# Performance work log

Measured on AMD Instinct MI355X. Metric: run time of the kernel, lower is better.

Reference implementation:

```python
import jax, jax.numpy as jnp
import numpy as np

N_NODES = 100000
N_EDGES = 1600000
D_IN, D_HID, D_OUT = 256, 128, 64


def setup_inputs() -> dict:
    key = jax.random.key(0)
    k = jax.random.split(key, 6)
    x = jax.random.normal(k[0], (N_NODES, D_IN), dtype=jnp.float32)
    edge_index = jax.random.randint(k[1], (2, N_EDGES), 0, N_NODES, dtype=jnp.int64)
    W1 = jax.random.normal(k[2], (D_IN, D_HID), dtype=jnp.float32) / np.sqrt(D_IN)
    b1 = jnp.zeros((D_HID,), dtype=jnp.float32)
    W2 = jax.random.normal(k[3], (D_HID, D_OUT), dtype=jnp.float32) / np.sqrt(D_HID)
    b2 = jnp.zeros((D_OUT,), dtype=jnp.float32)
    return {"x": x, "edge_index": edge_index, "W1": W1, "b1": b1, "W2": W2, "b2": b2}


def gcn_conv(x, W, b, src, dst, n):
    """PyG GCNConv: h = D^-1/2 (A+I) D^-1/2 (x W) + b, symmetric norm with self-loops."""
    h = x @ W                                           # [n, d_out]
    # degree from destination (col) index, +1 for the self-loop edge weight
    deg = jnp.ones((n,), x.dtype).at[dst].add(jnp.float32(1.0))
    dinv = jax.lax.rsqrt(deg)                           # deg >= 1, no inf
    norm = dinv[src] * dinv[dst]                        # [E]
    agg = jax.ops.segment_sum(h[src] * norm[:, None], dst, num_segments=n)
    agg = agg + h * (dinv * dinv)[:, None]              # self-loop contribution
    return agg + b


def reference(x, edge_index, W1, b1, W2, b2):
    src, dst = edge_index[0], edge_index[1]
    n = x.shape[0]
    h = gcn_conv(x, W1, b1, src, dst, n)
    h = jax.nn.relu(h)                                  # dropout is identity in eval mode
    out = gcn_conv(h, W2, b2, src, dst, n)
    return out
```

## Files before the change

kernel.cpp:

```cpp
#include <hip/hip_runtime.h>
#include <stdint.h>

typedef unsigned short u16;
typedef unsigned int u32;
typedef __bf16 bf16x8 __attribute__((ext_vector_type(8)));
typedef float floatx4 __attribute__((ext_vector_type(4)));

static __device__ __forceinline__ float bf2f(u16 u) {
  union { u32 i; float f; } v; v.i = ((u32)u) << 16; return v.f;
}
static __device__ __forceinline__ u16 f2bf(float f) {
  union { float f; u32 i; } v; v.f = f;
  u32 u = v.i;
  return (u16)((u + 0x7fffu + ((u >> 16) & 1u)) >> 16);
}

static __device__ __forceinline__ void gload_lds16(const void* g, void* l) {
  __builtin_amdgcn_global_load_lds(
      (const __attribute__((address_space(1))) void*)g,
      (__attribute__((address_space(3))) void*)l, 16, 0, 0);
}

__global__ void k_edgemode(const int* __restrict__ ei, int* __restrict__ flag) {
  int t = threadIdx.x;
  int v = ei[2 * t + 1];
  unsigned long long b = __ballot(v == 0);
  if (t == 0) *flag = (b == ~0ull) ? 1 : 0;
}

static __device__ __forceinline__ int edge_src(const int* ei, int E, int i, int m64) {
  return m64 ? ei[2 * (size_t)i] : ei[i];
}
static __device__ __forceinline__ int edge_dst(const int* ei, int E, int i, int m64) {
  return m64 ? ei[2 * (size_t)E + 2 * (size_t)i] : ei[(size_t)E + i];
}

__global__ void k_transpose(const float* __restrict__ W1, const float* __restrict__ W2,
                            u16* __restrict__ Wt1, u16* __restrict__ Wt2) {
  int i = blockIdx.x * 256 + threadIdx.x;
  if (i < 256 * 128) {
    int k = i >> 7, c = i & 127;
    Wt1[c * 256 + k] = f2bf(W1[i]);
  } else {
    int j = i - 256 * 128;
    if (j < 128 * 64) {
      int k = j >> 6, c = j & 63;
      Wt2[c * 128 + k] = f2bf(W2[j]);
    }
  }
}

#define CHUNK 2048

__global__ void k_count(const int* __restrict__ ei, int E, const int* __restrict__ flag,
                        int* __restrict__ bucket_cnt, int NB) {
  __shared__ int h[1024];
  const int t = threadIdx.x;
  for (int i = t; i < 1024; i += 256) h[i] = 0;
  __syncthreads();
  const int c0 = blockIdx.x * CHUNK;
  const int cnt = min(CHUNK, E - c0);
  const int m64 = *flag;
  for (int i = t; i < cnt; i += 256)
    atomicAdd(&h[edge_dst(ei, E, c0 + i, m64) >> 7], 1);
  __syncthreads();
  for (int i = t; i < NB; i += 256)
    if (h[i]) atomicAdd(&bucket_cnt[i], h[i]);
}

__global__ void k_bscan(const int* __restrict__ bucket_cnt, int* __restrict__ bucket_base,
                        int* __restrict__ bucket_cursor, int NB,
                        int* __restrict__ row_ptr, int n, int E) {
  __shared__ int ts[256];
  const int t = threadIdx.x;
  const int b4 = t * 4;
  int a0 = (b4 + 0 < NB) ? bucket_cnt[b4 + 0] : 0;
  int a1 = (b4 + 1 < NB) ? bucket_cnt[b4 + 1] : 0;
  int a2 = (b4 + 2 < NB) ? bucket_cnt[b4 + 2] : 0;
  int a3 = (b4 + 3 < NB) ? bucket_cnt[b4 + 3] : 0;
  int p1 = a0, p2 = p1 + a1, p3 = p2 + a2, tsum = p3 + a3;
  ts[t] = tsum;
  __syncthreads();
  for (int off = 1; off < 256; off <<= 1) {
    int x = (t >= off) ? ts[t - off] : 0;
    __syncthreads();
    ts[t] += x;
    __syncthreads();
  }
  int ex0 = ts[t] - tsum;
  int e[4] = {ex0, ex0 + p1, ex0 + p2, ex0 + p3};
#pragma unroll
  for (int j = 0; j < 4; ++j) {
    int i = b4 + j;
    if (i < NB) { bucket_base[i] = e[j]; bucket_cursor[i] = e[j]; }
  }
  if (t == 0) row_ptr[n] = E + n;
}

__global__ void k_place(const int* __restrict__ ei, int E, const int* __restrict__ flag,
                        int* __restrict__ bucket_cursor, uint2* __restrict__ pairs, int NB) {
  __shared__ int h[1024];
  __shared__ int ex[1024];
  __shared__ int cur[1024];
  __shared__ int ts[256];
  __shared__ uint2 stage[CHUNK];
  const int t = threadIdx.x;
  const int c0 = blockIdx.x * CHUNK;
  const int cnt = min(CHUNK, E - c0);
  const int m64 = *flag;

  for (int i = t; i < 1024; i += 256) h[i] = 0;
  __syncthreads();

  int es[8], ed[8];
#pragma unroll
  for (int j = 0; j < 8; ++j) {
    int i = t + j * 256;
    es[j] = 0; ed[j] = -1;
    if (i < cnt) {
      es[j] = edge_src(ei, E, c0 + i, m64);
      ed[j] = edge_dst(ei, E, c0 + i, m64);
      atomicAdd(&h[ed[j] >> 7], 1);
    }
  }
  __syncthreads();

  const int b4 = t * 4;
  int a0 = h[b4], a1 = h[b4 + 1], a2 = h[b4 + 2], a3 = h[b4 + 3];
  int p1 = a0, p2 = p1 + a1, p3 = p2 + a2, tsum = p3 + a3;
  ts[t] = tsum;
  __syncthreads();
  for (int off = 1; off < 256; off <<= 1) {
    int x = (t >= off) ? ts[t - off] : 0;
    __syncthreads();
    ts[t] += x;
    __syncthreads();
  }
  int ex0 = ts[t] - tsum;
  ex[b4] = ex0;       cur[b4] = ex0;
  ex[b4 + 1] = ex0 + p1; cur[b4 + 1] = ex0 + p1;
  ex[b4 + 2] = ex0 + p2; cur[b4 + 2] = ex0 + p2;
  ex[b4 + 3] = ex0 + p3; cur[b4 + 3] = ex0 + p3;
  __syncthreads();

#pragma unroll
  for (int j = 0; j < 8; ++j) {
    if (ed[j] >= 0) {
      int b = ed[j] >> 7;
      int pos = atomicAdd(&cur[b], 1);
      stage[pos] = make_uint2((u32)es[j], (u32)ed[j]);
    }
  }
  __syncthreads();
  for (int i = t; i < NB; i += 256) {
    int c = h[i];
    if (c > 0) h[i] = atomicAdd(&bucket_cursor[i], c);
  }
  __syncthreads();

  for (int i = t; i < cnt; i += 256) {
    uint2 p = stage[i];
    int b = (int)(p.y >> 7);
    pairs[h[b] + (i - ex[b])] = p;
  }
}

#define BMAX 3072
__global__ void k_csr(const uint2* __restrict__ pairs, const int* __restrict__ bucket_cnt,
                      const int* __restrict__ bucket_base, int* __restrict__ row_ptr,
                      float* __restrict__ dinv, int* __restrict__ srcs, int n) {
  __shared__ int h[128], cur[128];
  __shared__ int lsrc[BMAX];
  const int b = blockIdx.x;
  const int t = threadIdx.x;
  const int cnt = bucket_cnt[b];
  const int base = bucket_base[b];
  const int nbase = base + b * 128;

  if (t < 128) h[t] = 0;
  __syncthreads();
  for (int i = t; i < cnt; i += 256)
    atomicAdd(&h[pairs[base + i].y & 127], 1);
  __syncthreads();

  __shared__ int sc[128];
  int v = 0;
  if (t < 128) { v = h[t]; sc[t] = v; }
  __syncthreads();
  for (int off = 1; off < 128; off <<= 1) {
    int x = 0;
    if (t < 128 && t >= off) x = sc[t - off];
    __syncthreads();
    if (t < 128) sc[t] += x;
    __syncthreads();
  }
  if (t < 128) {
    int excl = sc[t] - v;
    cur[t] = excl + t + 1;
    int node = b * 128 + t;
    if (node < n) {
      row_ptr[node] = nbase + excl + t;
      dinv[node] = rsqrtf(1.0f + (float)v);
      int sp = excl + t;
      if (sp < BMAX) lsrc[sp] = node;
      else srcs[nbase + sp] = node;
    }
  }
  __syncthreads();

  for (int i = t; i < cnt; i += 256) {
    uint2 p = pairs[base + i];
    int pos = atomicAdd(&cur[p.y & 127], 1);
    if (pos < BMAX) lsrc[pos] = (int)p.x;
    else srcs[nbase + pos] = (int)p.x;
  }
  __syncthreads();
  const int lim = min(cnt + 128, BMAX);
  for (int i = t; i < lim; i += 256) srcs[nbase + i] = lsrc[i];
}

template<int N, int K, int CHK, bool A_FP32>
__launch_bounds__(256, 4)
__global__ void k_gemm(const void* __restrict__ Ap, const u16* __restrict__ Wt,
                       const float* __restrict__ dinv, u16* __restrict__ G, int M)
{
  constexpr int ESZ  = A_FP32 ? 4 : 2;
  constexpr int BPR  = K * ESZ;
  constexpr int BPRC = CHK * ESZ;
  constexpr int RPI  = 1024 / BPRC;
  constexpr int NISS = 64 / RPI;
  constexpr int STRIDE = 1024 + 16;
  constexpr int NCH  = K / CHK;
  constexpr int KSC  = CHK / 32;
  constexpr int IPW  = NISS / 4;
  constexpr int LPR  = BPRC / 16;
  __shared__ char lds[NISS * STRIDE];
  const int t = threadIdx.x;
  const int wave = t >> 6, lane = t & 63;
  const int row0 = blockIdx.x * 64;

  const int wr = wave >> 1, wc = wave & 1;
  constexpr int NT = N / 32;
  const int lm = lane & 15, lq = lane >> 4;

  floatx4 acc[2][NT];
#pragma unroll
  for (int i = 0; i < 2; ++i)
#pragma unroll
    for (int j = 0; j < NT; ++j) acc[i][j] = (floatx4)(0.0f);

  const int arow = wr * 32 + lm;
  const int brow0 = wc * (N / 2) + lm;

  for (int kc = 0; kc < NCH; ++kc) {
    const int kb = kc * BPRC;

#pragma unroll
    for (int i = 0; i < IPW; ++i) {
      const int g = wave * IPW + i;
      int r0 = row0 + g * RPI;
      if (r0 < M) {
        if (r0 > M - RPI) r0 = M - RPI;
        const char* src = (const char*)Ap + (size_t)r0 * BPR + kb
                          + (lane / LPR) * BPR + (lane % LPR) * 16;
        gload_lds16(src, lds + g * STRIDE);
      }
    }
    __syncthreads();

#pragma unroll
    for (int ksl = 0; ksl < KSC; ++ksl) {
      const int ks = kc * KSC + ksl;
      bf16x8 a[2];
#pragma unroll
      for (int mt = 0; mt < 2; ++mt) {
        const int r = arow + mt * 16;
        const char* p = lds + (r / RPI) * STRIDE + (r % RPI) * BPRC
                        + (ksl * 32 + lq * 8) * ESZ;
        if constexpr (A_FP32) {
          float4 f0 = *(const float4*)p;
          float4 f1 = *(const float4*)(p + 16);
          bf16x8 av;
          av[0] = (__bf16)f0.x; av[1] = (__bf16)f0.y; av[2] = (__bf16)f0.z; av[3] = (__bf16)f0.w;
          av[4] = (__bf16)f1.x; av[5] = (__bf16)f1.y; av[6] = (__bf16)f1.z; av[7] = (__bf16)f1.w;
          a[mt] = av;
        } else {
          a[mt] = *(const bf16x8*)p;
        }
      }
      bf16x8 b[NT];
#pragma unroll
      for (int nt = 0; nt < NT; ++nt)
        b[nt] = *(const bf16x8*)(Wt + (size_t)(brow0 + nt * 16) * K + ks * 32 + lq * 8);
#pragma unroll
      for (int nt = 0; nt < NT; ++nt) {
        acc[0][nt] = __builtin_amdgcn_mfma_f32_16x16x32_bf16(a[0], b[nt], acc[0][nt], 0, 0, 0);
        acc[1][nt] = __builtin_amdgcn_mfma_f32_16x16x32_bf16(a[1], b[nt], acc[1][nt], 0, 0, 0);
      }
    }
    __syncthreads();
  }

  const int crow0 = row0 + wr * 32 + lq * 4;
#pragma unroll
  for (int mt = 0; mt < 2; ++mt) {
#pragma unroll
    for (int nt = 0; nt < NT; ++nt) {
      const int gc = wc * (N / 2) + nt * 16 + lm;
#pragma unroll
      for (int r = 0; r < 4; ++r) {
        const int gr = crow0 + mt * 16 + r;
        if (gr < M) G[(size_t)gr * N + gc] = f2bf(acc[mt][nt][r] * dinv[gr]);
      }
    }
  }
}

template<int F, bool RELU, bool OUT_BF16, int NPW>
__launch_bounds__(256, 4)
__global__ void k_agg(const u16* __restrict__ g, const int* __restrict__ row_ptr,
                      const int* __restrict__ srcs, const float* __restrict__ dinv,
                      const float* __restrict__ bias, void* __restrict__ outp, int n)
{
  const int wid = blockIdx.x * 4 + (threadIdx.x >> 6);
  const int n0 = wid * NPW;
  if (n0 >= n) return;
  const int n1 = min(n0 + NPW, n);
  const int lane = threadIdx.x & 63;
  constexpr int VPL = F / 64;
  const int col = lane * VPL;
  const float b0 = bias[col];
  const float b1 = (VPL == 2) ? bias[col + (VPL - 1)] : 0.f;

  int e    = __builtin_amdgcn_readfirstlane(row_ptr[n0]);
  int eEnd = __builtin_amdgcn_readfirstlane(row_ptr[n1]);
  int cur  = n0;
  int nb   = __builtin_amdgcn_readfirstlane(row_ptr[n0 + 1]);
  float dv = dinv[n0];
  float a0 = 0.f, a1 = 0.f;

  auto fin = [&]() {
    float o0 = dv * a0 + b0;
    if (RELU) o0 = fmaxf(o0, 0.f);
    if constexpr (VPL == 2) {
      float o1 = dv * a1 + b1;
      if (RELU) o1 = fmaxf(o1, 0.f);
      if constexpr (OUT_BF16) {
        u32 pk = (u32)f2bf(o0) | ((u32)f2bf(o1) << 16);
        *(u32*)((u16*)outp + (size_t)cur * F + col) = pk;
      } else {
        *(float2*)((float*)outp + (size_t)cur * F + col) = make_float2(o0, o1);
      }
    } else {
      if constexpr (OUT_BF16) ((u16*)outp)[(size_t)cur * F + col] = f2bf(o0);
      else                    ((float*)outp)[(size_t)cur * F + col] = o0;
    }
    ++cur;
    a0 = 0.f; a1 = 0.f;
    if (cur < n) {
      dv = dinv[cur];
      nb = __builtin_amdgcn_readfirstlane(row_ptr[cur + 1]);
    }
  };

  auto issue = [&](int eb, u32* gv) {
    const int* sp = srcs + eb;
#pragma unroll
    for (int j = 0; j < 8; ++j) {
      const int s = sp[j];
      if constexpr (VPL == 2)
        gv[j] = *(const u32*)(g + (size_t)s * F + col);
      else
        gv[j] = (u32)g[(size_t)s * F + col];
    }
  };

  auto consume = [&](int eb, const u32* gv) {
#pragma unroll
    for (int j = 0; j < 8; ++j) {
      if (eb + j == nb) fin();
      if constexpr (VPL == 2) {
        a0 += bf2f((u16)gv[j]);
        a1 += bf2f((u16)(gv[j] >> 16));
      } else {
        a0 += bf2f((u16)gv[j]);
      }
    }
  };

  u32 gvA[8], gvB[8];
  const int rem = (eEnd - e) >> 3;
  if (rem >= 1) issue(e, gvA);
  if (rem >= 2) issue(e + 8, gvB);
  int i = 0;
  for (; i + 2 < rem; i += 2) {
    consume(e + i * 8, gvA);
    issue(e + (i + 2) * 8, gvA);
    consume(e + (i + 1) * 8, gvB);
    if (i + 3 < rem) issue(e + (i + 3) * 8, gvB);
  }
  if (i < rem) { consume(e + i * 8, gvA); ++i; }
  if (i < rem) { consume(e + i * 8, gvB); ++i; }

  for (int et = e + rem * 8; et < eEnd; ++et) {
    const int s = srcs[et];
    u32 gvt;
    if constexpr (VPL == 2) gvt = *(const u32*)(g + (size_t)s * F + col);
    else                    gvt = (u32)g[(size_t)s * F + col];
    if (et == nb) fin();
    if constexpr (VPL == 2) { a0 += bf2f((u16)gvt); a1 += bf2f((u16)(gvt >> 16)); }
    else                    a0 += bf2f((u16)gvt);
  }
  fin();
}

extern "C" void kernel_launch(void* const* d_in, const int* in_sizes, int n_in,
                              void* d_out, int out_size, void* d_ws, size_t ws_size,
                              hipStream_t stream)
{
  const float* x  = (const float*)d_in[0];
  const int*   ei = (const int*)d_in[1];
  const float* W1 = (const float*)d_in[2];
  const float* b1 = (const float*)d_in[3];
  const float* W2 = (const float*)d_in[4];
  const float* b2 = (const float*)d_in[5];

  const int n = in_sizes[0] / 256;
  const int E = in_sizes[1] / 2;
  const int NB = (n + 127) >> 7;

  char* ws = (char*)d_ws;
  size_t off = 0;
  auto alloc = [&](size_t bytes) -> void* {
    void* p = ws + off;
    off = (off + bytes + 255) & ~(size_t)255;
    return p;
  };
  int*   row_ptr = (int*)alloc((size_t)(n + 1) * 4);
  int*   bcnt    = (int*)alloc(1024 * 4);
  int*   bbase   = (int*)alloc(1024 * 4);
  int*   bcur    = (int*)alloc(1024 * 4);
  int*   eflag   = (int*)alloc(256);
  float* dinv    = (float*)alloc((size_t)n * 4);
  u16*   Wt1     = (u16*)alloc(256 * 128 * 2);
  u16*   Wt2     = (u16*)alloc(128 * 64 * 2);
  uint2* pairs   = (uint2*)alloc((size_t)E * 8);
  int*   srcs    = (int*)alloc((size_t)(E + n + 512) * 4);
  u16*   g1      = (u16*)alloc((size_t)n * 128 * 2);
  u16*   y1      = (u16*)alloc((size_t)n * 128 * 2);
  u16*   g2      = (u16*)alloc((size_t)n * 64 * 2);
  (void)ws_size; (void)n_in; (void)out_size;

  const int TB = 256;
  const int nbC = (E + CHUNK - 1) / CHUNK;

  hipMemsetAsync(bcnt, 0, 1024 * 4, stream);
  k_edgemode<<<1, 64, 0, stream>>>(ei, eflag);
  k_transpose<<<(256 * 128 + 128 * 64 + TB - 1) / TB, TB, 0, stream>>>(W1, W2, Wt1, Wt2);
  k_count<<<nbC, TB, 0, stream>>>(ei, E, eflag, bcnt, NB);
  k_bscan<<<1, TB, 0, stream>>>(bcnt, bbase, bcur, NB, row_ptr, n, E);
  k_place<<<nbC, TB, 0, stream>>>(ei, E, eflag, bcur, pairs, NB);
  k_csr<<<NB, TB, 0, stream>>>(pairs, bcnt, bbase, row_ptr, dinv, srcs, n);

  constexpr int NPW = 8;
  const int nwaves = (n + NPW - 1) / NPW;
  const int aggGrid = (nwaves + 3) / 4;

  k_gemm<128, 256, 128, true><<<(n + 63) / 64, 256, 0, stream>>>(x, Wt1, dinv, g1, n);
  k_agg<128, true, true, NPW><<<aggGrid, 256, 0, stream>>>(g1, row_ptr, srcs, dinv, b1, y1, n);
  k_gemm<64, 128, 128, false><<<(n + 63) / 64, 256, 0, stream>>>(y1, Wt2, dinv, g2, n);
  k_agg<64, false, false, NPW><<<aggGrid, 256, 0, stream>>>(g2, row_ptr, srcs, dinv, b2, d_out, n);
}
```

Measured before the change: 381.2 us.

## Load GEMM A operand directly from global memory instead of staging through LDS

The GEMM kernel no longer stages A-matrix chunks into shared memory with global_load_lds and barriers. Each lane now reads its A fragments straight from global memory into registers, and the K loop is fully unrolled. This removes the LDS traffic and the __syncthreads stalls, and frees shared memory, which may raise occupancy. In exchange, A reads become less coalesced (each lane fetches 16-32 strided bytes per row) and there is no explicit prefetch, so latency hiding relies on the compiler's scheduling of the unrolled loads.

```diff
diff --git a/kernel.cpp b/kernel.cpp
--- a/kernel.cpp
+++ b/kernel.cpp
@@ -13,12 +13,6 @@
   union { float f; u32 i; } v; v.f = f;
   u32 u = v.i;
   return (u16)((u + 0x7fffu + ((u >> 16) & 1u)) >> 16);
-}
-
-static __device__ __forceinline__ void gload_lds16(const void* g, void* l) {
-  __builtin_amdgcn_global_load_lds(
-      (const __attribute__((address_space(1))) void*)g,
-      (__attribute__((address_space(3))) void*)l, 16, 0, 0);
 }
 
 __global__ void k_edgemode(const int* __restrict__ ei, int* __restrict__ flag) {
@@ -219,28 +213,18 @@
   for (int i = t; i < lim; i += 256) srcs[nbase + i] = lsrc[i];
 }
 
-template<int N, int K, int CHK, bool A_FP32>
+template<int N, int K, bool A_FP32>
 __launch_bounds__(256, 4)
 __global__ void k_gemm(const void* __restrict__ Ap, const u16* __restrict__ Wt,
                        const float* __restrict__ dinv, u16* __restrict__ G, int M)
 {
-  constexpr int ESZ  = A_FP32 ? 4 : 2;
-  constexpr int BPR  = K * ESZ;
-  constexpr int BPRC = CHK * ESZ;
-  constexpr int RPI  = 1024 / BPRC;
-  constexpr int NISS = 64 / RPI;
-  constexpr int STRIDE = 1024 + 16;
-  constexpr int NCH  = K / CHK;
-  constexpr int KSC  = CHK / 32;
-  constexpr int IPW  = NISS / 4;
-  constexpr int LPR  = BPRC / 16;
-  __shared__ char lds[NISS * STRIDE];
+  constexpr int ESZ = A_FP32 ? 4 : 2;
+  constexpr int KS  = K / 32;
+  constexpr int NT  = N / 32;
   const int t = threadIdx.x;
   const int wave = t >> 6, lane = t & 63;
   const int row0 = blockIdx.x * 64;
-
   const int wr = wave >> 1, wc = wave & 1;
-  constexpr int NT = N / 32;
   const int lm = lane & 15, lq = lane >> 4;
 
   floatx4 acc[2][NT];
@@ -249,56 +233,41 @@
 #pragma unroll
     for (int j = 0; j < NT; ++j) acc[i][j] = (floatx4)(0.0f);
 
-  const int arow = wr * 32 + lm;
-  const int brow0 = wc * (N / 2) + lm;
-
-  for (int kc = 0; kc < NCH; ++kc) {
-    const int kb = kc * BPRC;
-
-#pragma unroll
-    for (int i = 0; i < IPW; ++i) {
-      const int g = wave * IPW + i;
-      int r0 = row0 + g * RPI;
-      if (r0 < M) {
-        if (r0 > M - RPI) r0 = M - RPI;
-        const char* src = (const char*)Ap + (size_t)r0 * BPR + kb
-                          + (lane / LPR) * BPR + (lane % LPR) * 16;
-        gload_lds16(src, lds + g * STRIDE);
-      }
-    }
-    __syncthreads();
-
-#pragma unroll
-    for (int ksl = 0; ksl < KSC; ++ksl) {
-      const int ks = kc * KSC + ksl;
-      bf16x8 a[2];
-#pragma unroll
-      for (int mt = 0; mt < 2; ++mt) {
-        const int r = arow + mt * 16;
-        const char* p = lds + (r / RPI) * STRIDE + (r % RPI) * BPRC
-                        + (ksl * 32 + lq * 8) * ESZ;
-        if constexpr (A_FP32) {
-          float4 f0 = *(const float4*)p;
-          float4 f1 = *(const float4*)(p + 16);
-          bf16x8 av;
-          av[0] = (__bf16)f0.x; av[1] = (__bf16)f0.y; av[2] = (__bf16)f0.z; av[3] = (__bf16)f0.w;
-          av[4] = (__bf16)f1.x; av[5] = (__bf16)f1.y; av[6] = (__bf16)f1.z; av[7] = (__bf16)f1.w;
-          a[mt] = av;
-        } else {
-          a[mt] = *(const bf16x8*)p;
-        }
-      }
-      bf16x8 b[NT];
-#pragma unroll
-      for (int nt = 0; nt < NT; ++nt)
-        b[nt] = *(const bf16x8*)(Wt + (size_t)(brow0 + nt * 16) * K + ks * 32 + lq * 8);
-#pragma unroll
-      for (int nt = 0; nt < NT; ++nt) {
-        acc[0][nt] = __builtin_amdgcn_mfma_f32_16x16x32_bf16(a[0], b[nt], acc[0][nt], 0, 0, 0);
-        acc[1][nt] = __builtin_amdgcn_mfma_f32_16x16x32_bf16(a[1], b[nt], acc[1][nt], 0, 0, 0);
-      }
-    }
-    __syncthreads();
+  int r0 = row0 + wr * 32 + lm;
+  int r1 = r0 + 16;
+  if (r0 >= M) r0 = M - 1;
+  if (r1 >= M) r1 = M - 1;
+  const char* pa0 = (const char*)Ap + ((size_t)r0 * K + lq * 8) * ESZ;
+  const char* pa1 = (const char*)Ap + ((size_t)r1 * K + lq * 8) * ESZ;
+  const u16*  pb  = Wt + (size_t)(wc * (N / 2) + lm) * K + lq * 8;
+
+#pragma unroll
+  for (int ks = 0; ks < KS; ++ks) {
+    bf16x8 a[2];
+    if constexpr (A_FP32) {
+      float4 f0 = *(const float4*)(pa0 + ks * 128);
+      float4 f1 = *(const float4*)(pa0 + ks * 128 + 16);
+      float4 g0 = *(const float4*)(pa1 + ks * 128);
+      float4 g1 = *(const float4*)(pa1 + ks * 128 + 16);
+      bf16x8 av, bv;
+      av[0] = (__bf16)f0.x; av[1] = (__bf16)f0.y; av[2] = (__bf16)f0.z; av[3] = (__bf16)f0.w;
+      av[4] = (__bf16)f1.x; av[5] = (__bf16)f1.y; av[6] = (__bf16)f1.z; av[7] = (__bf16)f1.w;
+      bv[0] = (__bf16)g0.x; bv[1] = (__bf16)g0.y; bv[2] = (__bf16)g0.z; bv[3] = (__bf16)g0.w;
+      bv[4] = (__bf16)g1.x; bv[5] = (__bf16)g1.y; bv[6] = (__bf16)g1.z; bv[7] = (__bf16)g1.w;
+      a[0] = av; a[1] = bv;
+    } else {
+      a[0] = *(const bf16x8*)(pa0 + ks * 64);
+      a[1] = *(const bf16x8*)(pa1 + ks * 64);
+    }
+    bf16x8 b[NT];
+#pragma unroll
+    for (int nt = 0; nt < NT; ++nt)
+      b[nt] = *(const bf16x8*)(pb + (size_t)nt * 16 * K + ks * 32);
+#pragma unroll
+    for (int nt = 0; nt < NT; ++nt) {
+      acc[0][nt] = __builtin_amdgcn_mfma_f32_16x16x32_bf16(a[0], b[nt], acc[0][nt], 0, 0, 0);
+      acc[1][nt] = __builtin_amdgcn_mfma_f32_16x16x32_bf16(a[1], b[nt], acc[1][nt], 0, 0, 0);
+    }
   }
 
   const int crow0 = row0 + wr * 32 + lq * 4;
@@ -466,8 +435,8 @@
   const int nwaves = (n + NPW - 1) / NPW;
   const int aggGrid = (nwaves + 3) / 4;
 
-  k_gemm<128, 256, 128, true><<<(n + 63) / 64, 256, 0, stream>>>(x, Wt1, dinv, g1, n);
+  k_gemm<128, 256, true><<<(n + 63) / 64, 256, 0, stream>>>(x, Wt1, dinv, g1, n);
   k_agg<128, true, true, NPW><<<aggGrid, 256, 0, stream>>>(g1, row_ptr, srcs, dinv, b1, y1, n);
-  k_gemm<64, 128, 128, false><<<(n + 63) / 64, 256, 0, stream>>>(y1, Wt2, dinv, g2, n);
+  k_gemm<64, 128, false><<<(n + 63) / 64, 256, 0, stream>>>(y1, Wt2, dinv, g2, n);
   k_agg<64, false, false, NPW><<<aggGrid, 256, 0, stream>>>(g2, row_ptr, srcs, dinv, b2, d_out, n);
 }
```

New measurement: 398.3 us. +4.5%, slower.

## Double-buffer GEMM LDS staging with swizzle and register-prefetched weights

Applied to the files above, without the earlier changes.

Restructures the GEMM K-loop so the LDS tile is double-buffered: the global-to-LDS load for the next chunk is issued before the current chunk is computed, with explicit vmcnt waits and raw barriers in place of __syncthreads. Adds an XOR swizzle on LDS columns to reduce bank conflicts, and preloads each chunk's weight fragments into registers ahead of the MFMA loop. The K chunk size is halved so the two buffers fit in LDS. This raises LDS use and register pressure, which may lower occupancy, and relies on the hand-written waitcnt accounting being correct.

```diff
diff --git a/kernel.cpp b/kernel.cpp
--- a/kernel.cpp
+++ b/kernel.cpp
@@ -234,49 +234,73 @@
   constexpr int KSC  = CHK / 32;
   constexpr int IPW  = NISS / 4;
   constexpr int LPR  = BPRC / 16;
-  __shared__ char lds[NISS * STRIDE];
+  constexpr int SWM  = 8 / RPI;
+  constexpr int NT   = N / 32;
+  __shared__ char lds[2 * NISS * STRIDE];
   const int t = threadIdx.x;
   const int wave = t >> 6, lane = t & 63;
   const int row0 = blockIdx.x * 64;
-
   const int wr = wave >> 1, wc = wave & 1;
-  constexpr int NT = N / 32;
   const int lm = lane & 15, lq = lane >> 4;
 
-  floatx4 acc[2][NT];
-#pragma unroll
-  for (int i = 0; i < 2; ++i)
-#pragma unroll
-    for (int j = 0; j < NT; ++j) acc[i][j] = (floatx4)(0.0f);
-
-  const int arow = wr * 32 + lm;
-  const int brow0 = wc * (N / 2) + lm;
-
-  for (int kc = 0; kc < NCH; ++kc) {
-    const int kb = kc * BPRC;
-
+  const int ril  = lane / LPR;
+  const int scol = ((lane % LPR) ^ (ril * SWM)) * 16;
+
+  auto stage = [&](int kc) {
+    char* buf = lds + (size_t)(kc & 1) * (NISS * STRIDE);
+    const size_t kb = (size_t)kc * BPRC;
 #pragma unroll
     for (int i = 0; i < IPW; ++i) {
       const int g = wave * IPW + i;
       int r0 = row0 + g * RPI;
       if (r0 < M) {
         if (r0 > M - RPI) r0 = M - RPI;
-        const char* src = (const char*)Ap + (size_t)r0 * BPR + kb
-                          + (lane / LPR) * BPR + (lane % LPR) * 16;
-        gload_lds16(src, lds + g * STRIDE);
-      }
-    }
-    __syncthreads();
-
+        gload_lds16((const char*)Ap + (size_t)(r0 + ril) * BPR + kb + scol,
+                    buf + g * STRIDE);
+      }
+    }
+  };
+
+  floatx4 acc[2][NT];
+#pragma unroll
+  for (int i = 0; i < 2; ++i)
+#pragma unroll
+    for (int j = 0; j < NT; ++j) acc[i][j] = (floatx4)(0.0f);
+
+  const int arow = wr * 32 + lm;
+  const u16* pb = Wt + (size_t)(wc * (N / 2) + lm) * K + lq * 8;
+
+  stage(0);
+
+#pragma unroll
+  for (int c = 0; c < NCH; ++c) {
+    bf16x8 breg[KSC][NT];
+#pragma unroll
+    for (int ksl = 0; ksl < KSC; ++ksl)
+#pragma unroll
+      for (int nt = 0; nt < NT; ++nt)
+        breg[ksl][nt] = *(const bf16x8*)(pb + (size_t)nt * 16 * K + (c * KSC + ksl) * 32);
+
+    if (c + 1 < NCH) {
+      stage(c + 1);
+      asm volatile("s_waitcnt vmcnt(%0)" :: "i"(IPW) : "memory");
+    } else {
+      asm volatile("s_waitcnt vmcnt(0)" ::: "memory");
+    }
+    __builtin_amdgcn_sched_barrier(0);
+    __builtin_amdgcn_s_barrier();
+    __builtin_amdgcn_sched_barrier(0);
+
+    const char* buf = lds + (size_t)(c & 1) * (NISS * STRIDE);
 #pragma unroll
     for (int ksl = 0; ksl < KSC; ++ksl) {
-      const int ks = kc * KSC + ksl;
       bf16x8 a[2];
 #pragma unroll
       for (int mt = 0; mt < 2; ++mt) {
         const int r = arow + mt * 16;
-        const char* p = lds + (r / RPI) * STRIDE + (r % RPI) * BPRC
-                        + (ksl * 32 + lq * 8) * ESZ;
+        const int cb = (ksl * 32 + lq * 8) * ESZ;
+        const char* p = buf + (r / RPI) * STRIDE + (r % RPI) * BPRC
+                        + (cb ^ ((r % RPI) * SWM * 16));
         if constexpr (A_FP32) {
           float4 f0 = *(const float4*)p;
           float4 f1 = *(const float4*)(p + 16);
@@ -288,17 +312,14 @@
           a[mt] = *(const bf16x8*)p;
         }
       }
-      bf16x8 b[NT];
-#pragma unroll
-      for (int nt = 0; nt < NT; ++nt)
-        b[nt] = *(const bf16x8*)(Wt + (size_t)(brow0 + nt * 16) * K + ks * 32 + lq * 8);
 #pragma unroll
       for (int nt = 0; nt < NT; ++nt) {
-        acc[0][nt] = __builtin_amdgcn_mfma_f32_16x16x32_bf16(a[0], b[nt], acc[0][nt], 0, 0, 0);
-        acc[1][nt] = __builtin_amdgcn_mfma_f32_16x16x32_bf16(a[1], b[nt], acc[1][nt], 0, 0, 0);
-      }
-    }
-    __syncthreads();
+        acc[0][nt] = __builtin_amdgcn_mfma_f32_16x16x32_bf16(a[0], breg[ksl][nt], acc[0][nt], 0, 0, 0);
+        acc[1][nt] = __builtin_amdgcn_mfma_f32_16x16x32_bf16(a[1], breg[ksl][nt], acc[1][nt], 0, 0, 0);
+      }
+    }
+    __builtin_amdgcn_sched_barrier(0);
+    __builtin_amdgcn_s_barrier();
   }
 
   const int crow0 = row0 + wr * 32 + lq * 4;
@@ -466,8 +487,8 @@
   const int nwaves = (n + NPW - 1) / NPW;
   const int aggGrid = (nwaves + 3) / 4;
 
-  k_gemm<128, 256, 128, true><<<(n + 63) / 64, 256, 0, stream>>>(x, Wt1, dinv, g1, n);
+  k_gemm<128, 256, 64, true><<<(n + 63) / 64, 256, 0, stream>>>(x, Wt1, dinv, g1, n);
   k_agg<128, true, true, NPW><<<aggGrid, 256, 0, stream>>>(g1, row_ptr, srcs, dinv, b1, y1, n);
-  k_gemm<64, 128, 128, false><<<(n + 63) / 64, 256, 0, stream>>>(y1, Wt2, dinv, g2, n);
+  k_gemm<64, 128, 64, false><<<(n + 63) / 64, 256, 0, stream>>>(y1, Wt2, dinv, g2, n);
   k_agg<64, false, false, NPW><<<aggGrid, 256, 0, stream>>>(g2, row_ptr, srcs, dinv, b2, d_out, n);
 }
```

Result: no change. 375.0 us (-1.6%).

## Restructure GEMM into per-wave triple-buffered pipeline with swizzled LDS and prefetched weights

Applied to the files above, without the earlier changes.

Rewrites the dense GEMM kernel so that each wave owns 32 rows and all N columns, with a private triple-buffered LDS region filled by async global-to-LDS loads two K-chunks ahead. Block-wide __syncthreads are replaced with per-wave vmcnt waits. The LDS layout uses an XOR swizzle to avoid bank conflicts, and weight fragments are double-buffered in registers. The aggregation kernel's occupancy hint is raised to 8 blocks, which adds register pressure and relies on tuned vmcnt counts being correct.

```diff
diff --git a/kernel.cpp b/kernel.cpp
--- a/kernel.cpp
+++ b/kernel.cpp
@@ -219,94 +219,107 @@
   for (int i = t; i < lim; i += 256) srcs[nbase + i] = lsrc[i];
 }
 
-template<int N, int K, int CHK, bool A_FP32>
-__launch_bounds__(256, 4)
+template<int N, int K, bool A_FP32>
+__launch_bounds__(256, A_FP32 ? 3 : 4)
 __global__ void k_gemm(const void* __restrict__ Ap, const u16* __restrict__ Wt,
                        const float* __restrict__ dinv, u16* __restrict__ G, int M)
 {
   constexpr int ESZ  = A_FP32 ? 4 : 2;
-  constexpr int BPR  = K * ESZ;
+  constexpr int CHK  = 32;
+  constexpr int NCH  = K / CHK;
   constexpr int BPRC = CHK * ESZ;
   constexpr int RPI  = 1024 / BPRC;
-  constexpr int NISS = 64 / RPI;
-  constexpr int STRIDE = 1024 + 16;
-  constexpr int NCH  = K / CHK;
-  constexpr int KSC  = CHK / 32;
-  constexpr int IPW  = NISS / 4;
+  constexpr int NISS = 32 / RPI;
   constexpr int LPR  = BPRC / 16;
-  __shared__ char lds[NISS * STRIDE];
+  constexpr int NT   = N / 16;
+  constexpr int CB   = 32 * BPRC;
+  constexpr int BPR  = K * ESZ;
+  __shared__ char lds[4 * 3 * CB];
   const int t = threadIdx.x;
   const int wave = t >> 6, lane = t & 63;
-  const int row0 = blockIdx.x * 64;
-
-  const int wr = wave >> 1, wc = wave & 1;
-  constexpr int NT = N / 32;
+  const int wrow = blockIdx.x * 128 + wave * 32;
+  if (wrow >= M) return;
+  char* mylds = lds + wave * (3 * CB);
   const int lm = lane & 15, lq = lane >> 4;
 
+  const int ril  = lane / LPR;
+  const int scol = ((lane % LPR) ^ (ril & (LPR - 1))) * 16;
+  const char* abase = (const char*)Ap;
+
+  auto stage = [&](int c) {
+#pragma unroll
+    for (int i = 0; i < NISS; ++i) {
+      int r0 = wrow + i * RPI;
+      if (r0 > M - RPI) r0 = M - RPI;
+      gload_lds16(abase + (size_t)(r0 + ril) * BPR + (size_t)c * BPRC + scol,
+                  mylds + (c % 3) * CB + i * 1024);
+    }
+  };
+
+  bf16x8 breg[2][NT];
+  auto loadB = [&](int c) {
+#pragma unroll
+    for (int nt = 0; nt < NT; ++nt)
+      breg[c & 1][nt] = *(const bf16x8*)(Wt + (size_t)(nt * 16 + lm) * K + c * CHK + lq * 8);
+  };
+
   floatx4 acc[2][NT];
 #pragma unroll
   for (int i = 0; i < 2; ++i)
 #pragma unroll
     for (int j = 0; j < NT; ++j) acc[i][j] = (floatx4)(0.0f);
 
-  const int arow = wr * 32 + lm;
-  const int brow0 = wc * (N / 2) + lm;
-
-  for (int kc = 0; kc < NCH; ++kc) {
-    const int kb = kc * BPRC;
-
-#pragma unroll
-    for (int i = 0; i < IPW; ++i) {
-      const int g = wave * IPW + i;
-      int r0 = row0 + g * RPI;
-      if (r0 < M) {
-        if (r0 > M - RPI) r0 = M - RPI;
-        const char* src = (const char*)Ap + (size_t)r0 * BPR + kb
-                          + (lane / LPR) * BPR + (lane % LPR) * 16;
-        gload_lds16(src, lds + g * STRIDE);
+  stage(0);
+  loadB(0);
+  stage(1);
+  asm volatile("s_waitcnt vmcnt(%0)" :: "i"(NISS) : "memory");
+  __builtin_amdgcn_sched_barrier(0);
+
+#pragma unroll
+  for (int c = 0; c < NCH; ++c) {
+    if (c + 1 < NCH) loadB(c + 1);
+    __builtin_amdgcn_sched_barrier(0);
+    if (c + 2 < NCH) stage(c + 2);
+    __builtin_amdgcn_sched_barrier(0);
+
+    bf16x8 a[2];
+#pragma unroll
+    for (int mt = 0; mt < 2; ++mt) {
+      const int lr = mt * 16 + lm;
+      const char* p = mylds + (c % 3) * CB + (lr / RPI) * 1024 + (lr % RPI) * BPRC;
+      if constexpr (A_FP32) {
+        const int k0 = lr & 7;
+        float4 f0 = *(const float4*)(p + (((lq * 2)     ^ k0) * 16));
+        float4 f1 = *(const float4*)(p + (((lq * 2 + 1) ^ k0) * 16));
+        bf16x8 av;
+        av[0] = (__bf16)f0.x; av[1] = (__bf16)f0.y; av[2] = (__bf16)f0.z; av[3] = (__bf16)f0.w;
+        av[4] = (__bf16)f1.x; av[5] = (__bf16)f1.y; av[6] = (__bf16)f1.z; av[7] = (__bf16)f1.w;
+        a[mt] = av;
+      } else {
+        const int k0 = lr & 3;
+        a[mt] = *(const bf16x8*)(p + ((lq ^ k0) * 16));
       }
     }
-    __syncthreads();
-
-#pragma unroll
-    for (int ksl = 0; ksl < KSC; ++ksl) {
-      const int ks = kc * KSC + ksl;
-      bf16x8 a[2];
-#pragma unroll
-      for (int mt = 0; mt < 2; ++mt) {
-        const int r = arow + mt * 16;
-        const char* p = lds + (r / RPI) * STRIDE + (r % RPI) * BPRC
-                        + (ksl * 32 + lq * 8) * ESZ;
-        if constexpr (A_FP32) {
-          float4 f0 = *(const float4*)p;
-          float4 f1 = *(const float4*)(p + 16);
-          bf16x8 av;
-          av[0] = (__bf16)f0.x; av[1] = (__bf16)f0.y; av[2] = (__bf16)f0.z; av[3] = (__bf16)f0.w;
-          av[4] = (__bf16)f1.x; av[5] = (__bf16)f1.y; av[6] = (__bf16)f1.z; av[7] = (__bf16)f1.w;
-          a[mt] = av;
-        } else {
-          a[mt] = *(const bf16x8*)p;
-        }
-      }
-      bf16x8 b[NT];
-#pragma unroll
-      for (int nt = 0; nt < NT; ++nt)
-        b[nt] = *(const bf16x8*)(Wt + (size_t)(brow0 + nt * 16) * K + ks * 32 + lq * 8);
-#pragma unroll
-      for (int nt = 0; nt < NT; ++nt) {
-        acc[0][nt] = __builtin_amdgcn_mfma_f32_16x16x32_bf16(a[0], b[nt], acc[0][nt], 0, 0, 0);
-        acc[1][nt] = __builtin_amdgcn_mfma_f32_16x16x32_bf16(a[1], b[nt], acc[1][nt], 0, 0, 0);
-      }
-    }
-    __syncthreads();
-  }
-
-  const int crow0 = row0 + wr * 32 + lq * 4;
+#pragma unroll
+    for (int nt = 0; nt < NT; ++nt) {
+      acc[0][nt] = __builtin_amdgcn_mfma_f32_16x16x32_bf16(a[0], breg[c & 1][nt], acc[0][nt], 0, 0, 0);
+      acc[1][nt] = __builtin_amdgcn_mfma_f32_16x16x32_bf16(a[1], breg[c & 1][nt], acc[1][nt], 0, 0, 0);
+    }
+    __builtin_amdgcn_sched_barrier(0);
+    if (c + 2 < NCH) {
+      asm volatile("s_waitcnt vmcnt(%0)" :: "i"(NISS) : "memory");
+    } else if (c + 1 < NCH) {
+      asm volatile("s_waitcnt vmcnt(0)" ::: "memory");
+    }
+    __builtin_amdgcn_sched_barrier(0);
+  }
+
+  const int crow0 = wrow + lq * 4;
 #pragma unroll
   for (int mt = 0; mt < 2; ++mt) {
 #pragma unroll
     for (int nt = 0; nt < NT; ++nt) {
-      const int gc = wc * (N / 2) + nt * 16 + lm;
+      const int gc = nt * 16 + lm;
 #pragma unroll
       for (int r = 0; r < 4; ++r) {
         const int gr = crow0 + mt * 16 + r;
@@ -317,7 +330,7 @@
 }
 
 template<int F, bool RELU, bool OUT_BF16, int NPW>
-__launch_bounds__(256, 4)
+__launch_bounds__(256, 8)
 __global__ void k_agg(const u16* __restrict__ g, const int* __restrict__ row_ptr,
                       const int* __restrict__ srcs, const float* __restrict__ dinv,
                       const float* __restrict__ bias, void* __restrict__ outp, int n)
@@ -466,8 +479,8 @@
   const int nwaves = (n + NPW - 1) / NPW;
   const int aggGrid = (nwaves + 3) / 4;
 
-  k_gemm<128, 256, 128, true><<<(n + 63) / 64, 256, 0, stream>>>(x, Wt1, dinv, g1, n);
+  k_gemm<128, 256, true><<<(n + 127) / 128, 256, 0, stream>>>(x, Wt1, dinv, g1, n);
   k_agg<128, true, true, NPW><<<aggGrid, 256, 0, stream>>>(g1, row_ptr, srcs, dinv, b1, y1, n);
-  k_gemm<64, 128, 128, false><<<(n + 63) / 64, 256, 0, stream>>>(y1, Wt2, dinv, g2, n);
+  k_gemm<64, 128, false><<<(n + 127) / 128, 256, 0, stream>>>(y1, Wt2, dinv, g2, n);
   k_agg<64, false, false, NPW><<<aggGrid, 256, 0, stream>>>(g2, row_ptr, srcs, dinv, b2, d_out, n);
 }
```

Result: no change. 387.8 us (+1.7%).
